# Kernel tuning notes

Measured on AMD Instinct MI355X. Metric: run time of the kernel, lower is better.

## Reference

```python
import jax, jax.numpy as jnp
import numpy as np
from jax import lax

# Straight-through sign: forward sign(x), backward passes grad where |x|<=1 (hardtanh STE)
@jax.custom_vjp
def sign_ste(x):
    return jnp.sign(x)

def _sign_fwd(x):
    return jnp.sign(x), x

def _sign_bwd(x, g):
    return (g * (jnp.abs(x) <= 1.0).astype(g.dtype),)

sign_ste.defvjp(_sign_fwd, _sign_bwd)

STRIDE = 1
PADDING = 1

def setup_inputs() -> dict:
    key = jax.random.key(0)
    k1, k2, k3 = jax.random.split(key, 3)
    B, Cin, H, W = 32, 256, 56, 56
    Cout, K = 256, 3
    inp = jax.random.normal(k1, (B, Cin, H, W), dtype=jnp.float32)
    # kaiming-uniform-ish init like torch Conv2d default
    fan_in = Cin * K * K
    bound = 1.0 / np.sqrt(fan_in)
    weight1 = jax.random.uniform(k2, (Cout, Cin, K, K), minval=-bound, maxval=bound, dtype=jnp.float32)
    weight2 = jax.random.uniform(k3, (Cout, Cin, K, K), minval=-bound, maxval=bound, dtype=jnp.float32)
    return {"input": inp, "weight1": weight1, "weight2": weight2}

def reference(input, weight1, weight2):
    # ternarized weight: (sign(w1)+sign(w2))/2 in {-1,-0.5,0,0.5,1}
    w_ter = (sign_ste(weight1) + sign_ste(weight2)) * 0.5
    x_bin = sign_ste(input)
    out = lax.conv_general_dilated(
        x_bin, w_ter,
        window_strides=(STRIDE, STRIDE),
        padding=[(PADDING, PADDING), (PADDING, PADDING)],
        dimension_numbers=("NCHW", "OIHW", "NCHW"),
    )
    # per-output-channel scaling: mean|w1| + mean|w2| over (in, kh, kw)
    alpha = jnp.mean(jnp.abs(weight1), axis=(1, 2, 3)) + jnp.mean(jnp.abs(weight2), axis=(1, 2, 3))
    return out * alpha[None, :, None, None]
```

## Files before the change

kernel.cpp:

```cpp
#include <hip/hip_runtime.h>
#include <hip/hip_bf16.h>

#define B_    32
#define C_    256
#define H_    56
#define W_    56
#define HP    58
#define WPAD  58
#define HW    3136
#define CHW   802816
#define M_TOT 100352

typedef char  charx16 __attribute__((ext_vector_type(16)));
typedef int   intx4   __attribute__((ext_vector_type(4)));

#define XPAD_BYTES (B_ * HP * WPAD * C_)
#define WPK_BYTES  (C_ * 9 * C_)

__device__ __forceinline__ int sgn8(float f) {
  return ((f > 0.f) ? 1 : ((f < 0.f) ? -1 : 0)) & 0xff;
}

__global__ __launch_bounds__(256) void pack_w_kernel(const float* __restrict__ w1,
                                                     const float* __restrict__ w2,
                                                     char* __restrict__ wq,
                                                     float* __restrict__ alphah) {
  __shared__ float l1[2304], l2[2304];
  const int co = blockIdx.x;
  const int tid = threadIdx.x;
  const float* s1 = w1 + co * 2304;
  const float* s2 = w2 + co * 2304;
#pragma unroll
  for (int i = 0; i < 9; ++i) {
    l1[i * 256 + tid] = s1[i * 256 + tid];
    l2[i * 256 + tid] = s2[i * 256 + tid];
  }
  __syncthreads();
  const int ci = tid;
  float sabs = 0.f;
#pragma unroll
  for (int s = 0; s < 9; ++s) {
    const float a = l1[ci * 9 + s];
    const float b = l2[ci * 9 + s];
    const int sa = (a > 0.f) - (a < 0.f);
    const int sb = (b > 0.f) - (b < 0.f);
    wq[(co * 9 + s) * C_ + ci] = (char)(sa + sb);
    sabs += fabsf(a) + fabsf(b);
  }
#pragma unroll
  for (int off = 32; off > 0; off >>= 1) sabs += __shfl_down(sabs, off, 64);
  __shared__ float red[4];
  if ((tid & 63) == 0) red[tid >> 6] = sabs;
  __syncthreads();
  if (tid == 0)
    alphah[co] = (red[0] + red[1] + red[2] + red[3]) * (0.5f / 2304.0f);
}

#define ROWPC 272
__global__ __launch_bounds__(256) void pack_x_kernel(const float* __restrict__ in,
                                                     char* __restrict__ xp) {
  __shared__ char row[58 * ROWPC];
  const int yp = blockIdx.x % HP;
  const int b  = blockIdx.x / HP;
  const int tid = threadIdx.x;

  float4* rz = (float4*)row;
  const float4 z4 = make_float4(0.f, 0.f, 0.f, 0.f);
#pragma unroll
  for (int i = 0; i < 4; ++i) {
    const int idx = i * 256 + tid;
    if (idx < (58 * ROWPC) / 16) rz[idx] = z4;
  }
  __syncthreads();

  const int y = yp - 1;
  const int xq = tid % 14;
  const int cs = tid / 14;
  if (y >= 0 && y < H_ && cs < 18) {
    const float* base = in + ((size_t)b * C_ * H_ + (size_t)y) * W_ + xq * 4;
#pragma unroll
    for (int k = 0; k < 4; ++k) {
      const int cq = cs + 18 * k;
      if (cq < 64) {
        float4 f[4];
#pragma unroll
        for (int j = 0; j < 4; ++j)
          f[j] = *(const float4*)(base + (size_t)(cq * 4 + j) * (H_ * W_));
#pragma unroll
        for (int d = 0; d < 4; ++d) {
          const float v0 = (d == 0) ? f[0].x : (d == 1) ? f[0].y : (d == 2) ? f[0].z : f[0].w;
          const float v1 = (d == 0) ? f[1].x : (d == 1) ? f[1].y : (d == 2) ? f[1].z : f[1].w;
          const float v2 = (d == 0) ? f[2].x : (d == 1) ? f[2].y : (d == 2) ? f[2].z : f[2].w;
          const float v3 = (d == 0) ? f[3].x : (d == 1) ? f[3].y : (d == 2) ? f[3].z : f[3].w;
          const unsigned int pk = (unsigned)sgn8(v0) | ((unsigned)sgn8(v1) << 8) |
                                  ((unsigned)sgn8(v2) << 16) | ((unsigned)sgn8(v3) << 24);
          *(unsigned int*)&row[(xq * 4 + d + 1) * ROWPC + cq * 4] = pk;
        }
      }
    }
  }
  __syncthreads();

  const int cc = tid & 15;
  const int xo = tid >> 4;
  char* dst = xp + (size_t)(b * HP + yp) * WPAD * C_;
#pragma unroll
  for (int it = 0; it < 4; ++it) {
    const int xs = it * 16 + xo;
    if (xs < WPAD)
      *(float4*)(dst + xs * C_ + cc * 16) = *(const float4*)&row[xs * ROWPC + cc * 16];
  }
}

#define GLL16(src, dst)                                                        \
  __builtin_amdgcn_global_load_lds(                                            \
      (const __attribute__((address_space(1))) void*)(src),                    \
      (__attribute__((address_space(3))) void*)(dst), 16, 0, 0)

__global__ __launch_bounds__(512, 2) void gemm_kernel(const char* __restrict__ xp,
                                                      const char* __restrict__ wq,
                                                      const float* __restrict__ alphah,
                                                      float* __restrict__ out) {
  __shared__ char sA[3 * 128 * 128];
  __shared__ char sB[3 * 256 * 128];
  const int tid = threadIdx.x;

  const int id = blockIdx.x;
  const int xcd = id & 7;
  const int l = id >> 3;
  const int co0 = (l & 1) * 128;
  const int m0 = ((l >> 1) * 8 + xcd) * 256;

  const int srow = tid >> 3;
  const int scol = (tid & 7) ^ (srow & 7);

  const char* wsrc[2];
  const char* xsrc[4];
#pragma unroll
  for (int i = 0; i < 2; ++i)
    wsrc[i] = wq + (co0 + srow + 64 * i) * 9 * C_ + scol * 16;
#pragma unroll
  for (int i = 0; i < 4; ++i) {
    const int m = m0 + srow + 64 * i;
    const int b = m / HW;
    const int rem = m - b * HW;
    const int y = rem / W_;
    const int x = rem - y * W_;
    xsrc[i] = xp + ((b * HP + y) * WPAD + x) * C_ + scol * 16;
  }

  intx4 acc[4][4] = {};

  const int lane = tid & 63;
  const int wave = tid >> 6;
  const int wm = wave >> 2;
  const int wn = wave & 3;
  const int lrow = lane & 15;
  const int quad = lane >> 4;
  const int swk = lrow & 7;
  const int abase = (wm * 64 + lrow) * 128;
  const int bbase = (wn * 64 + lrow) * 128;

  auto stage = [&](int t, int bufi) {
    const int s = t >> 1;
    const int hh = (t & 1) * 128;
    const int woff = s * C_ + hh;
    const int shoff = ((s / 3) * WPAD + (s % 3)) * C_ + hh;
    char* dA = sA + bufi * 16384 + tid * 16;
    char* dB = sB + bufi * 32768 + tid * 16;
#pragma unroll
    for (int i = 0; i < 2; ++i)
      GLL16(wsrc[i] + woff, dA + i * 8192);
#pragma unroll
    for (int i = 0; i < 4; ++i)
      GLL16(xsrc[i] + shoff, dB + i * 8192);
  };

  stage(0, 0);
  asm volatile("" ::: "memory");
  stage(1, 1);

  int cb = 0;
  int cs = 2;
  for (int t = 0; t < 18; ++t) {
    if (t < 17)
      asm volatile("s_waitcnt vmcnt(6) lgkmcnt(0)" ::: "memory");
    else
      asm volatile("s_waitcnt vmcnt(0) lgkmcnt(0)" ::: "memory");
    __builtin_amdgcn_s_barrier();
    if (t < 16) stage(t + 2, cs);

    const char* bA = sA + cb * 16384;
    const char* bB = sB + cb * 32768;
#pragma unroll
    for (int kf = 0; kf < 2; ++kf) {
      const int coff = (((kf << 2) + quad) ^ swk) << 4;
      intx4 af[4], bfv[4];
#pragma unroll
      for (int i = 0; i < 4; ++i)
        af[i] = *(const intx4*)(bA + abase + i * 2048 + coff);
#pragma unroll
      for (int j = 0; j < 4; ++j)
        bfv[j] = *(const intx4*)(bB + bbase + j * 2048 + coff);
      __builtin_amdgcn_s_setprio(1);
#pragma unroll
      for (int i = 0; i < 4; ++i)
#pragma unroll
        for (int j = 0; j < 4; ++j)
          acc[i][j] = __builtin_amdgcn_mfma_i32_16x16x64_i8(af[i], bfv[j],
                                                            acc[i][j], 0, 0, 0);
      __builtin_amdgcn_s_setprio(0);
    }
    cb = (cb == 2) ? 0 : cb + 1;
    cs = (cs == 2) ? 0 : cs + 1;
  }

  int ob[4];
#pragma unroll
  for (int j = 0; j < 4; ++j) {
    const int m = m0 + wn * 64 + j * 16 + lrow;
    const int b = m / HW;
    const int rem = m - b * HW;
    const int y = rem / W_;
    const int x = rem - y * W_;
    ob[j] = b * CHW + y * W_ + x;
  }
#pragma unroll
  for (int i = 0; i < 4; ++i) {
#pragma unroll
    for (int r = 0; r < 4; ++r) {
      const int co = co0 + wm * 64 + i * 16 + quad * 4 + r;
      const float sc = alphah[co];
#pragma unroll
      for (int j = 0; j < 4; ++j)
        out[ob[j] + co * HW] = (float)acc[i][j][r] * sc;
    }
  }
}

extern "C" void kernel_launch(void* const* d_in, const int* in_sizes, int n_in,
                              void* d_out, int out_size, void* d_ws, size_t ws_size,
                              hipStream_t stream) {
  const float* input = (const float*)d_in[0];
  const float* w1 = (const float*)d_in[1];
  const float* w2 = (const float*)d_in[2];
  float* out = (float*)d_out;

  char* ws = (char*)d_ws;
  char* xp = ws;
  char* wq = ws + XPAD_BYTES;
  float* alphah = (float*)(ws + XPAD_BYTES + WPK_BYTES);

  pack_w_kernel<<<C_, 256, 0, stream>>>(w1, w2, wq, alphah);
  pack_x_kernel<<<B_ * HP, 256, 0, stream>>>(input, xp);
  gemm_kernel<<<(M_TOT / 256) * (C_ / 128), 512, 0, stream>>>(xp, wq, alphah, out);
}
```

Before: 283.6 us.

## Use 256x256 output tiles with quadrant-interleaved LDS staging pipeline

Each GEMM block now computes all 256 output channels for 256 pixels instead of 128 channels, halving the grid to 392 blocks and removing the redundant re-read of the activation tile by two blocks. The main loop splits each K-step into four quadrant sub-steps that interleave global-to-LDS loads of the next stage with MFMA work on the current one, using 128 KB of double-buffered LDS. This raises register pressure (128 accumulators per lane) and LDS use, which may cut occupancy to one block per CU, and adds many more barriers.

```diff
diff --git a/kernel.cpp b/kernel.cpp
--- a/kernel.cpp
+++ b/kernel.cpp
@@ -11,8 +11,7 @@
 #define CHW   802816
 #define M_TOT 100352
 
-typedef char  charx16 __attribute__((ext_vector_type(16)));
-typedef int   intx4   __attribute__((ext_vector_type(4)));
+typedef int intx4 __attribute__((ext_vector_type(4)));
 
 #define XPAD_BYTES (B_ * HP * WPAD * C_)
 #define WPK_BYTES  (C_ * 9 * C_)
@@ -117,102 +116,163 @@
       (const __attribute__((address_space(1))) void*)(src),                    \
       (__attribute__((address_space(3))) void*)(dst), 16, 0, 0)
 
+#define ENDBAR()                                                               \
+  do {                                                                         \
+    __builtin_amdgcn_s_barrier();                                              \
+    asm volatile("" ::: "memory");                                             \
+  } while (0)
+
+template <int PAR, int QM>
+__device__ __forceinline__ void load_a(const char* sA, int aoff, int c0, int c1,
+                                       intx4 (&a0)[4][2]) {
+  const char* ab = sA + PAR * 32768 + QM * 16384 + aoff;
+#pragma unroll
+  for (int ii = 0; ii < 4; ++ii) {
+    a0[ii][0] = *(const intx4*)(ab + ii * 2048 + c0);
+    a0[ii][1] = *(const intx4*)(ab + ii * 2048 + c1);
+  }
+}
+
+template <int PAR, int QN>
+__device__ __forceinline__ void load_b(const char* sB, int boff, int c0, int c1,
+                                       intx4 (&bv)[2][2]) {
+  const char* bb = sB + PAR * 32768 + QN * 16384 + boff;
+#pragma unroll
+  for (int jj = 0; jj < 2; ++jj) {
+    bv[jj][0] = *(const intx4*)(bb + jj * 2048 + c0);
+    bv[jj][1] = *(const intx4*)(bb + jj * 2048 + c1);
+  }
+}
+
+template <int QM, int QN>
+__device__ __forceinline__ void mfma_quad(intx4 (&a0)[4][2], intx4 (&bv)[2][2],
+                                          intx4 (&acc)[8][4]) {
+  __builtin_amdgcn_s_barrier();
+  asm volatile("s_waitcnt lgkmcnt(0)" ::: "memory");
+  __builtin_amdgcn_sched_barrier(0);
+  __builtin_amdgcn_s_setprio(1);
+#pragma unroll
+  for (int ii = 0; ii < 4; ++ii)
+#pragma unroll
+    for (int jj = 0; jj < 2; ++jj)
+#pragma unroll
+      for (int kf = 0; kf < 2; ++kf)
+        acc[QM * 4 + ii][QN * 2 + jj] = __builtin_amdgcn_mfma_i32_16x16x64_i8(
+            a0[ii][kf], bv[jj][kf], acc[QM * 4 + ii][QN * 2 + jj], 0, 0, 0);
+  __builtin_amdgcn_s_setprio(0);
+}
+
 __global__ __launch_bounds__(512, 2) void gemm_kernel(const char* __restrict__ xp,
                                                       const char* __restrict__ wq,
                                                       const float* __restrict__ alphah,
                                                       float* __restrict__ out) {
-  __shared__ char sA[3 * 128 * 128];
-  __shared__ char sB[3 * 256 * 128];
+  __shared__ char sA[65536];
+  __shared__ char sB[65536];
   const int tid = threadIdx.x;
 
   const int id = blockIdx.x;
-  const int xcd = id & 7;
-  const int l = id >> 3;
-  const int co0 = (l & 1) * 128;
-  const int m0 = ((l >> 1) * 8 + xcd) * 256;
-
-  const int srow = tid >> 3;
-  const int scol = (tid & 7) ^ (srow & 7);
-
-  const char* wsrc[2];
-  const char* xsrc[4];
-#pragma unroll
-  for (int i = 0; i < 2; ++i)
-    wsrc[i] = wq + (co0 + srow + 64 * i) * 9 * C_ + scol * 16;
-#pragma unroll
-  for (int i = 0; i < 4; ++i) {
-    const int m = m0 + srow + 64 * i;
-    const int b = m / HW;
-    const int rem = m - b * HW;
-    const int y = rem / W_;
-    const int x = rem - y * W_;
-    xsrc[i] = xp + ((b * HP + y) * WPAD + x) * C_ + scol * 16;
-  }
-
-  intx4 acc[4][4] = {};
+  const int m0 = ((id & 7) * 49 + (id >> 3)) * 256;
+
+  const int rg = tid >> 3;
+  const int cgs = ((tid & 7) ^ (rg & 7)) * 16;
+
+  const char* aw[2][2];
+  const char* xb[2][2];
+#pragma unroll
+  for (int h = 0; h < 2; ++h) {
+#pragma unroll
+    for (int g = 0; g < 2; ++g) {
+      const int r = rg + g * 64;
+      const int co = (g == 0) ? (h * 64 + r) : (128 + h * 64 + (r - 64));
+      aw[h][g] = wq + co * 2304 + cgs;
+      const int m = m0 + (r >> 5) * 64 + h * 32 + (r & 31);
+      const int b = m / HW;
+      const int rem = m - b * HW;
+      const int y = rem / W_;
+      const int x = rem - y * W_;
+      xb[h][g] = xp + ((b * HP + y) * WPAD + x) * C_ + cgs;
+    }
+  }
+  char* const dA = sA + tid * 16;
+  char* const dB = sB + tid * 16;
+
+  auto stageA = [&](int s, int h) {
+    if (s > 17) return;
+    const int tap = s >> 1, ph = s & 1;
+    const int off = tap * 256 + ph * 128;
+    char* d = dA + ph * 32768 + h * 16384;
+    GLL16(aw[h][0] + off, d);
+    GLL16(aw[h][1] + off, d + 8192);
+  };
+  auto stageB = [&](int s, int h) {
+    if (s > 17) return;
+    const int tap = s >> 1, ph = s & 1;
+    const int off = ((tap / 3) * WPAD + (tap % 3)) * C_ + ph * 128;
+    char* d = dB + ph * 32768 + h * 16384;
+    GLL16(xb[h][0] + off, d);
+    GLL16(xb[h][1] + off, d + 8192);
+  };
 
   const int lane = tid & 63;
   const int wave = tid >> 6;
   const int wm = wave >> 2;
   const int wn = wave & 3;
   const int lrow = lane & 15;
-  const int quad = lane >> 4;
-  const int swk = lrow & 7;
-  const int abase = (wm * 64 + lrow) * 128;
-  const int bbase = (wn * 64 + lrow) * 128;
-
-  auto stage = [&](int t, int bufi) {
-    const int s = t >> 1;
-    const int hh = (t & 1) * 128;
-    const int woff = s * C_ + hh;
-    const int shoff = ((s / 3) * WPAD + (s % 3)) * C_ + hh;
-    char* dA = sA + bufi * 16384 + tid * 16;
-    char* dB = sB + bufi * 32768 + tid * 16;
-#pragma unroll
-    for (int i = 0; i < 2; ++i)
-      GLL16(wsrc[i] + woff, dA + i * 8192);
-#pragma unroll
-    for (int i = 0; i < 4; ++i)
-      GLL16(xsrc[i] + shoff, dB + i * 8192);
-  };
-
-  stage(0, 0);
-  asm volatile("" ::: "memory");
-  stage(1, 1);
-
-  int cb = 0;
-  int cs = 2;
-  for (int t = 0; t < 18; ++t) {
-    if (t < 17)
-      asm volatile("s_waitcnt vmcnt(6) lgkmcnt(0)" ::: "memory");
-    else
-      asm volatile("s_waitcnt vmcnt(0) lgkmcnt(0)" ::: "memory");
-    __builtin_amdgcn_s_barrier();
-    if (t < 16) stage(t + 2, cs);
-
-    const char* bA = sA + cb * 16384;
-    const char* bB = sB + cb * 32768;
-#pragma unroll
-    for (int kf = 0; kf < 2; ++kf) {
-      const int coff = (((kf << 2) + quad) ^ swk) << 4;
-      intx4 af[4], bfv[4];
-#pragma unroll
-      for (int i = 0; i < 4; ++i)
-        af[i] = *(const intx4*)(bA + abase + i * 2048 + coff);
-#pragma unroll
-      for (int j = 0; j < 4; ++j)
-        bfv[j] = *(const intx4*)(bB + bbase + j * 2048 + coff);
-      __builtin_amdgcn_s_setprio(1);
-#pragma unroll
-      for (int i = 0; i < 4; ++i)
-#pragma unroll
-        for (int j = 0; j < 4; ++j)
-          acc[i][j] = __builtin_amdgcn_mfma_i32_16x16x64_i8(af[i], bfv[j],
-                                                            acc[i][j], 0, 0, 0);
-      __builtin_amdgcn_s_setprio(0);
-    }
-    cb = (cb == 2) ? 0 : cb + 1;
-    cs = (cs == 2) ? 0 : cs + 1;
+  const int kq = lane >> 4;
+  const int c0 = ((kq) ^ (lrow & 7)) * 16;
+  const int c1 = ((4 + kq) ^ (lrow & 7)) * 16;
+  const int aoff = wm * 8192 + lrow * 128;
+  const int boff = wn * 4096 + lrow * 128;
+
+  intx4 a0[4][2], bv[2][2];
+  intx4 acc[8][4] = {};
+
+  stageA(0, 0); stageB(0, 0); stageA(0, 1); stageB(0, 1);
+  stageA(1, 0); stageB(1, 1);
+  asm volatile("s_waitcnt vmcnt(4)" ::: "memory");
+  ENDBAR();
+
+#pragma unroll 1
+  for (int i = 0; i < 9; ++i) {
+    const int s1 = 2 * i + 1, s2 = 2 * i + 2, s3 = 2 * i + 3;
+    load_a<0, 0>(sA, aoff, c0, c1, a0);
+    load_b<0, 0>(sB, boff, c0, c1, bv);
+    stageA(s1, 1);
+    mfma_quad<0, 0>(a0, bv, acc);
+    ENDBAR();
+    load_b<0, 1>(sB, boff, c0, c1, bv);
+    stageB(s1, 0);
+    mfma_quad<0, 1>(a0, bv, acc);
+    ENDBAR();
+    load_a<0, 1>(sA, aoff, c0, c1, a0);
+    stageA(s2, 0);
+    mfma_quad<1, 1>(a0, bv, acc);
+    ENDBAR();
+    load_b<0, 0>(sB, boff, c0, c1, bv);
+    stageB(s2, 1);
+    mfma_quad<1, 0>(a0, bv, acc);
+    if (i < 8) asm volatile("s_waitcnt vmcnt(4)" ::: "memory");
+    else       asm volatile("s_waitcnt vmcnt(0)" ::: "memory");
+    ENDBAR();
+    load_a<1, 0>(sA, aoff, c0, c1, a0);
+    load_b<1, 0>(sB, boff, c0, c1, bv);
+    stageA(s2, 1);
+    mfma_quad<0, 0>(a0, bv, acc);
+    ENDBAR();
+    load_b<1, 1>(sB, boff, c0, c1, bv);
+    stageB(s2, 0);
+    mfma_quad<0, 1>(a0, bv, acc);
+    ENDBAR();
+    load_a<1, 1>(sA, aoff, c0, c1, a0);
+    stageA(s3, 0);
+    mfma_quad<1, 1>(a0, bv, acc);
+    ENDBAR();
+    load_b<1, 0>(sB, boff, c0, c1, bv);
+    stageB(s3, 1);
+    mfma_quad<1, 0>(a0, bv, acc);
+    if (i < 8) asm volatile("s_waitcnt vmcnt(4)" ::: "memory");
+    else       asm volatile("s_waitcnt vmcnt(0)" ::: "memory");
+    ENDBAR();
   }
 
   int ob[4];
@@ -226,14 +286,14 @@
     ob[j] = b * CHW + y * W_ + x;
   }
 #pragma unroll
-  for (int i = 0; i < 4; ++i) {
+  for (int ii = 0; ii < 8; ++ii) {
 #pragma unroll
     for (int r = 0; r < 4; ++r) {
-      const int co = co0 + wm * 64 + i * 16 + quad * 4 + r;
+      const int co = wm * 128 + ii * 16 + kq * 4 + r;
       const float sc = alphah[co];
 #pragma unroll
       for (int j = 0; j < 4; ++j)
-        out[ob[j] + co * HW] = (float)acc[i][j][r] * sc;
+        out[ob[j] + co * HW] = (float)acc[ii][j][r] * sc;
     }
   }
 }
@@ -253,5 +313,5 @@
 
   pack_w_kernel<<<C_, 256, 0, stream>>>(w1, w2, wq, alphah);
   pack_x_kernel<<<B_ * HP, 256, 0, stream>>>(input, xp);
-  gemm_kernel<<<(M_TOT / 256) * (C_ / 128), 512, 0, stream>>>(xp, wq, alphah, out);
-}
+  gemm_kernel<<<392, 512, 0, stream>>>(xp, wq, alphah, out);
+}
```

Result: faster. 265.1 us (-6.5%).

## Merge pack kernels and retile int8 GEMM to 256 threads with double buffering

Applied to the files above, without the earlier changes.

Fuses the weight and input packing kernels into one launch, so weight blocks are appended after the input-row blocks and one launch is saved. The GEMM goes from 512 to 256 threads per block. Each wave now computes a 128x64 tile with 8x4 MFMA accumulators. The K step shrinks to 64 bytes and the pipeline becomes a 2-stage double buffer with a __syncthreads each of the 36 iterations. The aim is to cut LDS footprint and raise occupancy, at the cost of more barriers, more accumulator registers and less prefetch depth than the previous 3-stage pipeline.

```diff
diff --git a/kernel.cpp b/kernel.cpp
--- a/kernel.cpp
+++ b/kernel.cpp
@@ -11,8 +11,7 @@
 #define CHW   802816
 #define M_TOT 100352
 
-typedef char  charx16 __attribute__((ext_vector_type(16)));
-typedef int   intx4   __attribute__((ext_vector_type(4)));
+typedef int intx4 __attribute__((ext_vector_type(4)));
 
 #define XPAD_BYTES (B_ * HP * WPAD * C_)
 #define WPK_BYTES  (C_ * 9 * C_)
@@ -21,94 +20,97 @@
   return ((f > 0.f) ? 1 : ((f < 0.f) ? -1 : 0)) & 0xff;
 }
 
-__global__ __launch_bounds__(256) void pack_w_kernel(const float* __restrict__ w1,
-                                                     const float* __restrict__ w2,
-                                                     char* __restrict__ wq,
-                                                     float* __restrict__ alphah) {
-  __shared__ float l1[2304], l2[2304];
-  const int co = blockIdx.x;
+#define ROWPC 272
+__global__ __launch_bounds__(256) void pack_kernel(const float* __restrict__ in,
+                                                   const float* __restrict__ w1,
+                                                   const float* __restrict__ w2,
+                                                   char* __restrict__ xp,
+                                                   char* __restrict__ wq,
+                                                   float* __restrict__ alphah) {
+  __shared__ char smem[18448];
   const int tid = threadIdx.x;
-  const float* s1 = w1 + co * 2304;
-  const float* s2 = w2 + co * 2304;
-#pragma unroll
-  for (int i = 0; i < 9; ++i) {
-    l1[i * 256 + tid] = s1[i * 256 + tid];
-    l2[i * 256 + tid] = s2[i * 256 + tid];
-  }
-  __syncthreads();
-  const int ci = tid;
-  float sabs = 0.f;
-#pragma unroll
-  for (int s = 0; s < 9; ++s) {
-    const float a = l1[ci * 9 + s];
-    const float b = l2[ci * 9 + s];
-    const int sa = (a > 0.f) - (a < 0.f);
-    const int sb = (b > 0.f) - (b < 0.f);
-    wq[(co * 9 + s) * C_ + ci] = (char)(sa + sb);
-    sabs += fabsf(a) + fabsf(b);
-  }
-#pragma unroll
-  for (int off = 32; off > 0; off >>= 1) sabs += __shfl_down(sabs, off, 64);
-  __shared__ float red[4];
-  if ((tid & 63) == 0) red[tid >> 6] = sabs;
-  __syncthreads();
-  if (tid == 0)
-    alphah[co] = (red[0] + red[1] + red[2] + red[3]) * (0.5f / 2304.0f);
-}
-
-#define ROWPC 272
-__global__ __launch_bounds__(256) void pack_x_kernel(const float* __restrict__ in,
-                                                     char* __restrict__ xp) {
-  __shared__ char row[58 * ROWPC];
-  const int yp = blockIdx.x % HP;
-  const int b  = blockIdx.x / HP;
-  const int tid = threadIdx.x;
-
-  float4* rz = (float4*)row;
-  const float4 z4 = make_float4(0.f, 0.f, 0.f, 0.f);
-#pragma unroll
-  for (int i = 0; i < 4; ++i) {
-    const int idx = i * 256 + tid;
-    if (idx < (58 * ROWPC) / 16) rz[idx] = z4;
-  }
-  __syncthreads();
-
-  const int y = yp - 1;
-  const int xq = tid % 14;
-  const int cs = tid / 14;
-  if (y >= 0 && y < H_ && cs < 18) {
-    const float* base = in + ((size_t)b * C_ * H_ + (size_t)y) * W_ + xq * 4;
-#pragma unroll
-    for (int k = 0; k < 4; ++k) {
-      const int cq = cs + 18 * k;
-      if (cq < 64) {
-        float4 f[4];
-#pragma unroll
-        for (int j = 0; j < 4; ++j)
-          f[j] = *(const float4*)(base + (size_t)(cq * 4 + j) * (H_ * W_));
-#pragma unroll
-        for (int d = 0; d < 4; ++d) {
-          const float v0 = (d == 0) ? f[0].x : (d == 1) ? f[0].y : (d == 2) ? f[0].z : f[0].w;
-          const float v1 = (d == 0) ? f[1].x : (d == 1) ? f[1].y : (d == 2) ? f[1].z : f[1].w;
-          const float v2 = (d == 0) ? f[2].x : (d == 1) ? f[2].y : (d == 2) ? f[2].z : f[2].w;
-          const float v3 = (d == 0) ? f[3].x : (d == 1) ? f[3].y : (d == 2) ? f[3].z : f[3].w;
-          const unsigned int pk = (unsigned)sgn8(v0) | ((unsigned)sgn8(v1) << 8) |
-                                  ((unsigned)sgn8(v2) << 16) | ((unsigned)sgn8(v3) << 24);
-          *(unsigned int*)&row[(xq * 4 + d + 1) * ROWPC + cq * 4] = pk;
+
+  if (blockIdx.x < B_ * HP) {
+    char* row = smem;
+    const int yp = blockIdx.x % HP;
+    const int b  = blockIdx.x / HP;
+
+    float4* rz = (float4*)row;
+    const float4 z4 = make_float4(0.f, 0.f, 0.f, 0.f);
+#pragma unroll
+    for (int i = 0; i < 4; ++i) {
+      const int idx = i * 256 + tid;
+      if (idx < (58 * ROWPC) / 16) rz[idx] = z4;
+    }
+    __syncthreads();
+
+    const int y = yp - 1;
+    const int xq = tid % 14;
+    const int cs = tid / 14;
+    if (y >= 0 && y < H_ && cs < 18) {
+      const float* base = in + ((size_t)b * C_ * H_ + (size_t)y) * W_ + xq * 4;
+#pragma unroll
+      for (int k = 0; k < 4; ++k) {
+        const int cq = cs + 18 * k;
+        if (cq < 64) {
+          float4 f[4];
+#pragma unroll
+          for (int j = 0; j < 4; ++j)
+            f[j] = *(const float4*)(base + (size_t)(cq * 4 + j) * (H_ * W_));
+#pragma unroll
+          for (int d = 0; d < 4; ++d) {
+            const float v0 = (d == 0) ? f[0].x : (d == 1) ? f[0].y : (d == 2) ? f[0].z : f[0].w;
+            const float v1 = (d == 0) ? f[1].x : (d == 1) ? f[1].y : (d == 2) ? f[1].z : f[1].w;
+            const float v2 = (d == 0) ? f[2].x : (d == 1) ? f[2].y : (d == 2) ? f[2].z : f[2].w;
+            const float v3 = (d == 0) ? f[3].x : (d == 1) ? f[3].y : (d == 2) ? f[3].z : f[3].w;
+            const unsigned int pk = (unsigned)sgn8(v0) | ((unsigned)sgn8(v1) << 8) |
+                                    ((unsigned)sgn8(v2) << 16) | ((unsigned)sgn8(v3) << 24);
+            *(unsigned int*)&row[(xq * 4 + d + 1) * ROWPC + cq * 4] = pk;
+          }
         }
       }
     }
-  }
-  __syncthreads();
-
-  const int cc = tid & 15;
-  const int xo = tid >> 4;
-  char* dst = xp + (size_t)(b * HP + yp) * WPAD * C_;
-#pragma unroll
-  for (int it = 0; it < 4; ++it) {
-    const int xs = it * 16 + xo;
-    if (xs < WPAD)
-      *(float4*)(dst + xs * C_ + cc * 16) = *(const float4*)&row[xs * ROWPC + cc * 16];
+    __syncthreads();
+
+    const int cc = tid & 15;
+    const int xo = tid >> 4;
+    char* dst = xp + (size_t)(b * HP + yp) * WPAD * C_;
+#pragma unroll
+    for (int it = 0; it < 4; ++it) {
+      const int xs = it * 16 + xo;
+      if (xs < WPAD)
+        *(float4*)(dst + xs * C_ + cc * 16) = *(const float4*)&row[xs * ROWPC + cc * 16];
+    }
+  } else {
+    float* l1 = (float*)smem;
+    float* l2 = l1 + 2304;
+    float* red = (float*)(smem + 18432);
+    const int co = blockIdx.x - B_ * HP;
+    const float* s1 = w1 + co * 2304;
+    const float* s2 = w2 + co * 2304;
+#pragma unroll
+    for (int i = 0; i < 9; ++i) {
+      l1[i * 256 + tid] = s1[i * 256 + tid];
+      l2[i * 256 + tid] = s2[i * 256 + tid];
+    }
+    __syncthreads();
+    const int ci = tid;
+    float sabs = 0.f;
+#pragma unroll
+    for (int s = 0; s < 9; ++s) {
+      const float a = l1[ci * 9 + s];
+      const float b = l2[ci * 9 + s];
+      const int sa = (a > 0.f) - (a < 0.f);
+      const int sb = (b > 0.f) - (b < 0.f);
+      wq[(co * 9 + s) * C_ + ci] = (char)(sa + sb);
+      sabs += fabsf(a) + fabsf(b);
+    }
+#pragma unroll
+    for (int off = 32; off > 0; off >>= 1) sabs += __shfl_down(sabs, off, 64);
+    if ((tid & 63) == 0) red[tid >> 6] = sabs;
+    __syncthreads();
+    if (tid == 0)
+      alphah[co] = (red[0] + red[1] + red[2] + red[3]) * (0.5f / 2304.0f);
   }
 }
 
@@ -117,12 +119,12 @@
       (const __attribute__((address_space(1))) void*)(src),                    \
       (__attribute__((address_space(3))) void*)(dst), 16, 0, 0)
 
-__global__ __launch_bounds__(512, 2) void gemm_kernel(const char* __restrict__ xp,
+__global__ __launch_bounds__(256, 2) void gemm_kernel(const char* __restrict__ xp,
                                                       const char* __restrict__ wq,
                                                       const float* __restrict__ alphah,
                                                       float* __restrict__ out) {
-  __shared__ char sA[3 * 128 * 128];
-  __shared__ char sB[3 * 256 * 128];
+  __shared__ char sA[2 * 128 * 64];
+  __shared__ char sB[2 * 256 * 64];
   const int tid = threadIdx.x;
 
   const int id = blockIdx.x;
@@ -131,14 +133,14 @@
   const int co0 = (l & 1) * 128;
   const int m0 = ((l >> 1) * 8 + xcd) * 256;
 
-  const int srow = tid >> 3;
-  const int scol = (tid & 7) ^ (srow & 7);
+  const int srow = tid >> 2;
+  const int scol = (tid & 3) ^ ((tid >> 3) & 3);
 
   const char* wsrc[2];
+#pragma unroll
+  for (int i = 0; i < 2; ++i)
+    wsrc[i] = wq + (co0 + srow + 64 * i) * 2304 + scol * 16;
   const char* xsrc[4];
-#pragma unroll
-  for (int i = 0; i < 2; ++i)
-    wsrc[i] = wq + (co0 + srow + 64 * i) * 9 * C_ + scol * 16;
 #pragma unroll
   for (int i = 0; i < 4; ++i) {
     const int m = m0 + srow + 64 * i;
@@ -149,70 +151,53 @@
     xsrc[i] = xp + ((b * HP + y) * WPAD + x) * C_ + scol * 16;
   }
 
-  intx4 acc[4][4] = {};
+  auto stage = [&](int s) {
+    const int tap = s >> 2;
+    const int q = s & 3;
+    const int woff = tap * 256 + q * 64;
+    const int shoff = ((tap / 3) * WPAD + (tap % 3)) * C_ + q * 64;
+    char* dA = sA + (s & 1) * 8192 + tid * 16;
+    char* dB = sB + (s & 1) * 16384 + tid * 16;
+#pragma unroll
+    for (int i = 0; i < 2; ++i)
+      GLL16(wsrc[i] + woff, dA + i * 4096);
+#pragma unroll
+    for (int i = 0; i < 4; ++i)
+      GLL16(xsrc[i] + shoff, dB + i * 4096);
+  };
 
   const int lane = tid & 63;
-  const int wave = tid >> 6;
-  const int wm = wave >> 2;
-  const int wn = wave & 3;
+  const int wn = tid >> 6;
   const int lrow = lane & 15;
-  const int quad = lane >> 4;
-  const int swk = lrow & 7;
-  const int abase = (wm * 64 + lrow) * 128;
-  const int bbase = (wn * 64 + lrow) * 128;
-
-  auto stage = [&](int t, int bufi) {
-    const int s = t >> 1;
-    const int hh = (t & 1) * 128;
-    const int woff = s * C_ + hh;
-    const int shoff = ((s / 3) * WPAD + (s % 3)) * C_ + hh;
-    char* dA = sA + bufi * 16384 + tid * 16;
-    char* dB = sB + bufi * 32768 + tid * 16;
-#pragma unroll
-    for (int i = 0; i < 2; ++i)
-      GLL16(wsrc[i] + woff, dA + i * 8192);
-#pragma unroll
-    for (int i = 0; i < 4; ++i)
-      GLL16(xsrc[i] + shoff, dB + i * 8192);
-  };
-
-  stage(0, 0);
-  asm volatile("" ::: "memory");
-  stage(1, 1);
-
-  int cb = 0;
-  int cs = 2;
-  for (int t = 0; t < 18; ++t) {
-    if (t < 17)
-      asm volatile("s_waitcnt vmcnt(6) lgkmcnt(0)" ::: "memory");
-    else
-      asm volatile("s_waitcnt vmcnt(0) lgkmcnt(0)" ::: "memory");
-    __builtin_amdgcn_s_barrier();
-    if (t < 16) stage(t + 2, cs);
-
-    const char* bA = sA + cb * 16384;
-    const char* bB = sB + cb * 32768;
-#pragma unroll
-    for (int kf = 0; kf < 2; ++kf) {
-      const int coff = (((kf << 2) + quad) ^ swk) << 4;
-      intx4 af[4], bfv[4];
-#pragma unroll
-      for (int i = 0; i < 4; ++i)
-        af[i] = *(const intx4*)(bA + abase + i * 2048 + coff);
+  const int kq = lane >> 4;
+  const int coff = (kq ^ ((lrow >> 1) & 3)) * 16;
+  const int abase = lrow * 64 + coff;
+  const int bbase = (wn * 64 + lrow) * 64 + coff;
+
+  intx4 acc[8][4] = {};
+
+  stage(0);
+#pragma unroll 1
+  for (int t = 0; t < 36; ++t) {
+    __syncthreads();
+    if (t < 35) stage(t + 1);
+    const char* bA = sA + (t & 1) * 8192;
+    const char* bB = sB + (t & 1) * 16384;
+    intx4 af[8], bv[4];
+#pragma unroll
+    for (int ii = 0; ii < 8; ++ii)
+      af[ii] = *(const intx4*)(bA + abase + ii * 1024);
+#pragma unroll
+    for (int j = 0; j < 4; ++j)
+      bv[j] = *(const intx4*)(bB + bbase + j * 1024);
+    __builtin_amdgcn_s_setprio(1);
+#pragma unroll
+    for (int ii = 0; ii < 8; ++ii)
 #pragma unroll
       for (int j = 0; j < 4; ++j)
-        bfv[j] = *(const intx4*)(bB + bbase + j * 2048 + coff);
-      __builtin_amdgcn_s_setprio(1);
-#pragma unroll
-      for (int i = 0; i < 4; ++i)
-#pragma unroll
-        for (int j = 0; j < 4; ++j)
-          acc[i][j] = __builtin_amdgcn_mfma_i32_16x16x64_i8(af[i], bfv[j],
-                                                            acc[i][j], 0, 0, 0);
-      __builtin_amdgcn_s_setprio(0);
-    }
-    cb = (cb == 2) ? 0 : cb + 1;
-    cs = (cs == 2) ? 0 : cs + 1;
+        acc[ii][j] = __builtin_amdgcn_mfma_i32_16x16x64_i8(af[ii], bv[j],
+                                                           acc[ii][j], 0, 0, 0);
+    __builtin_amdgcn_s_setprio(0);
   }
 
   int ob[4];
@@ -226,14 +211,14 @@
     ob[j] = b * CHW + y * W_ + x;
   }
 #pragma unroll
-  for (int i = 0; i < 4; ++i) {
+  for (int ii = 0; ii < 8; ++ii) {
 #pragma unroll
     for (int r = 0; r < 4; ++r) {
-      const int co = co0 + wm * 64 + i * 16 + quad * 4 + r;
+      const int co = co0 + ii * 16 + kq * 4 + r;
       const float sc = alphah[co];
 #pragma unroll
       for (int j = 0; j < 4; ++j)
-        out[ob[j] + co * HW] = (float)acc[i][j][r] * sc;
+        out[ob[j] + co * HW] = (float)acc[ii][j][r] * sc;
     }
   }
 }
@@ -251,7 +236,6 @@
   char* wq = ws + XPAD_BYTES;
   float* alphah = (float*)(ws + XPAD_BYTES + WPK_BYTES);
 
-  pack_w_kernel<<<C_, 256, 0, stream>>>(w1, w2, wq, alphah);
-  pack_x_kernel<<<B_ * HP, 256, 0, stream>>>(input, xp);
-  gemm_kernel<<<(M_TOT / 256) * (C_ / 128), 512, 0, stream>>>(xp, wq, alphah, out);
-}
+  pack_kernel<<<B_ * HP + C_, 256, 0, stream>>>(input, w1, w2, xp, wq, alphah);
+  gemm_kernel<<<784, 256, 0, stream>>>(xp, wq, alphah, out);
+}
```

After: 259.6 us. 1.09x faster.
